# Kernel tuning notes

Measured on AMD Instinct MI355X. Metric: run time of the kernel, lower is better.

The kernel has to match this reference:

```python
import jax, jax.numpy as jnp
import numpy as np

B, Q, C = 16, 3000, 1203


def setup_inputs() -> dict:
    key = jax.random.key(0)
    k1, k2, k3, k4 = jax.random.split(key, 4)
    pred_logits = jax.random.normal(k1, (B, Q, C), dtype=jnp.float32)
    pred_boxes = jax.random.uniform(k2, (B, Q, 4), dtype=jnp.float32)
    target_sizes = jax.random.randint(k3, (B, 2), 0, 1333, dtype=jnp.int64)
    class_present = jax.random.randint(k4, (B, C), 0, 2) > 0  # bool [B, C]
    return {
        "pred_logits": pred_logits,
        "pred_boxes": pred_boxes,
        "target_sizes": target_sizes,
        "class_present": class_present,
    }


def reference(pred_logits, pred_boxes, target_sizes, class_present):
    # prob[b,q,c] = sigmoid(logits); keep if prob >= 0.5 * max_q prob[b,:,c]
    # AND class c is in targets[b]['labels'] (class_present mask).
    del target_sizes  # only shape-asserted in the original forward
    prob = jax.nn.sigmoid(pred_logits)                      # [B,Q,C]
    top = jnp.max(prob, axis=1, keepdims=True)              # [B,1,C]
    keep = (prob >= 0.5 * top) & class_present[:, None, :]   # [B,Q,C] bool
    scores = jnp.where(keep, prob, jnp.zeros((), prob.dtype))  # masked scores
    box_keep = jnp.any(keep, axis=2)                        # [B,Q] query kept for some class
    boxes = pred_boxes * box_keep[..., None].astype(pred_boxes.dtype)  # [B,Q,4]
    return scores, keep, boxes
```

## Files before the change

kernel.cpp:

```cpp
#include <hip/hip_runtime.h>
#include <math.h>

#define NB 16
#define NQR 3000
#define NC 1203

typedef float f32x4 __attribute__((ext_vector_type(4)));

__device__ __forceinline__ int lane_proc(float x, float t,
                                         float* __restrict__ s,
                                         float* __restrict__ k) {
    float pf = __builtin_amdgcn_rcpf(1.0f + __expf(-x));
    bool kp;
    float sc;
    if (pf > t + 1e-5f) {
        kp = true;  sc = pf;
    } else if (pf < t - 1e-5f) {
        kp = false; sc = 0.0f;
    } else {
        float e32 = (float)exp(-(double)x);
        float p32 = 1.0f / (1.0f + e32);
        kp = (p32 >= t);
        sc = kp ? p32 : 0.0f;
    }
    *s = sc;
    *k = kp ? 1.0f : 0.0f;
    return kp ? 1 : 0;
}

__global__ void k_partial_max(const float* __restrict__ logits,
                              float* __restrict__ partial,
                              int qc) {
    int c = blockIdx.x * blockDim.x + threadIdx.x;
    int b = blockIdx.y;
    int z = blockIdx.z;
    if (c >= NC) return;
    int q0 = z * qc;
    int q1 = min(NQR, q0 + qc);
    float m = -INFINITY;
    const float* p = logits + ((size_t)(b * NQR + q0)) * NC + c;
    int q = q0;
    for (; q + 4 <= q1; q += 4) {
        float a0 = p[0];
        float a1 = p[NC];
        float a2 = p[2 * NC];
        float a3 = p[3 * NC];
        m = fmaxf(m, fmaxf(fmaxf(a0, a1), fmaxf(a2, a3)));
        p += 4 * NC;
    }
    for (; q < q1; ++q) {
        m = fmaxf(m, *p);
        p += NC;
    }
    partial[((size_t)z * NB + b) * NC + c] = m;
}

__global__ void k_thresh(const float* __restrict__ partial,
                         const int* __restrict__ cls_present,
                         float* __restrict__ thrf,
                         int nz) {
    int c = blockIdx.x * blockDim.x + threadIdx.x;
    int b = blockIdx.y;
    if (c >= NC) return;
    float m = -INFINITY;
    for (int z = 0; z < nz; ++z)
        m = fmaxf(m, partial[((size_t)z * NB + b) * NC + c]);
    float t;
    if (cls_present[b * NC + c]) {
        float e32  = (float)exp(-(double)m);
        float ptop = 1.0f / (1.0f + e32);
        t = 0.5f * ptop;
    } else {
        t = INFINITY;
    }
    thrf[(size_t)b * NC + c] = t;
}

__global__ __launch_bounds__(256) void k_main(const float* __restrict__ logits,
                                              const float* __restrict__ boxes,
                                              const float* __restrict__ thrf,
                                              float* __restrict__ scores,
                                              float* __restrict__ keep,
                                              float* __restrict__ boxes_out) {
    int wid  = threadIdx.x >> 6;
    int lane = threadIdx.x & 63;
    int row  = blockIdx.x * 4 + wid;
    int b    = row / NQR;

    const float* lrow = logits + (size_t)row * NC;
    const float* tf   = thrf + (size_t)b * NC;
    float* srow = scores + (size_t)row * NC;
    float* krow = keep + (size_t)row * NC;

    int head = row & 3;
    int any = 0;
    float sv, kv;

    if (lane < head) {
        int c = lane;
        any |= lane_proc(lrow[c], tf[c], &sv, &kv);
        __builtin_nontemporal_store(sv, srow + c);
        __builtin_nontemporal_store(kv, krow + c);
    }

    for (int v = lane; v < 300; v += 64) {
        int c = head + 4 * v;
        f32x4 x4 = *(const f32x4*)(lrow + c);
        f32x4 s4, k4;
        float s0, s1, s2, s3, k0, k1, k2, k3;
        any |= lane_proc(x4.x, tf[c + 0], &s0, &k0);
        any |= lane_proc(x4.y, tf[c + 1], &s1, &k1);
        any |= lane_proc(x4.z, tf[c + 2], &s2, &k2);
        any |= lane_proc(x4.w, tf[c + 3], &s3, &k3);
        s4 = (f32x4){s0, s1, s2, s3};
        k4 = (f32x4){k0, k1, k2, k3};
        __builtin_nontemporal_store(s4, (f32x4*)(srow + c));
        __builtin_nontemporal_store(k4, (f32x4*)(krow + c));
    }

    if (lane < 3 - head) {
        int c = head + 1200 + lane;
        any |= lane_proc(lrow[c], tf[c], &sv, &kv);
        __builtin_nontemporal_store(sv, srow + c);
        __builtin_nontemporal_store(kv, krow + c);
    }

    unsigned long long m = __ballot(any);
    if (lane == 0) {
        float mm = m ? 1.0f : 0.0f;
        f32x4 bx = *(const f32x4*)(boxes + (size_t)row * 4);
        f32x4 o = bx * mm;
        *(f32x4*)(boxes_out + (size_t)row * 4) = o;
    }
}

extern "C" void kernel_launch(void* const* d_in, const int* in_sizes, int n_in,
                              void* d_out, int out_size, void* d_ws, size_t ws_size,
                              hipStream_t stream) {
    const float* logits      = (const float*)d_in[0];
    const float* boxes       = (const float*)d_in[1];
    const int*   cls_present = (const int*)d_in[3];

    float* scores    = (float*)d_out;
    float* keep      = scores + (size_t)NB * NQR * NC;
    float* boxes_out = keep + (size_t)NB * NQR * NC;

    int nz = 25;
    while (nz > 1 && ((size_t)nz + 1) * NB * NC * sizeof(float) > ws_size)
        nz /= 2;
    float* partial = (float*)d_ws;
    float* thrf    = partial + (size_t)nz * NB * NC;
    int qc = (NQR + nz - 1) / nz;

    dim3 gmax((NC + 255) / 256, NB, nz);
    k_partial_max<<<gmax, 256, 0, stream>>>(logits, partial, qc);

    dim3 gthr((NC + 255) / 256, NB);
    k_thresh<<<gthr, 256, 0, stream>>>(partial, cls_present, thrf, nz);

    k_main<<<(NB * NQR) / 4, 256, 0, stream>>>(logits, boxes, thrf,
                                               scores, keep, boxes_out);
}
```

Before: 190.5 us.

## Fuse column max, threshold and masking into one column-tiled kernel

Replaces the three-kernel pipeline (partial max, threshold, row-wise main pass) with one kernel per (16-column tile, batch). Each block reduces the column max over all queries in shared memory, computes thresholds, then re-reads its column strip to write scores and keep, so the second logits read can hit L2 and the extra launches disappear. The block index is remapped so consecutive column tiles land on the same XCD. Box outputs are zeroed by a separate kernel and written only for kept rows. Only 1216 blocks run, each doing scalar 64-byte-wide accesses instead of float4 rows, which risks lower bandwidth utilisation and occupancy.

```diff
diff --git a/kernel.cpp b/kernel.cpp
--- a/kernel.cpp
+++ b/kernel.cpp
@@ -28,109 +28,97 @@
     return kp ? 1 : 0;
 }
 
-__global__ void k_partial_max(const float* __restrict__ logits,
-                              float* __restrict__ partial,
-                              int qc) {
-    int c = blockIdx.x * blockDim.x + threadIdx.x;
-    int b = blockIdx.y;
-    int z = blockIdx.z;
-    if (c >= NC) return;
-    int q0 = z * qc;
-    int q1 = min(NQR, q0 + qc);
-    float m = -INFINITY;
-    const float* p = logits + ((size_t)(b * NQR + q0)) * NC + c;
-    int q = q0;
-    for (; q + 4 <= q1; q += 4) {
-        float a0 = p[0];
-        float a1 = p[NC];
-        float a2 = p[2 * NC];
-        float a3 = p[3 * NC];
-        m = fmaxf(m, fmaxf(fmaxf(a0, a1), fmaxf(a2, a3)));
-        p += 4 * NC;
-    }
-    for (; q < q1; ++q) {
-        m = fmaxf(m, *p);
-        p += NC;
-    }
-    partial[((size_t)z * NB + b) * NC + c] = m;
+__global__ void k_zero(float* __restrict__ p, int n) {
+    int i = blockIdx.x * 256 + threadIdx.x;
+    if (i < n) p[i] = 0.0f;
 }
 
-__global__ void k_thresh(const float* __restrict__ partial,
-                         const int* __restrict__ cls_present,
-                         float* __restrict__ thrf,
-                         int nz) {
-    int c = blockIdx.x * blockDim.x + threadIdx.x;
-    int b = blockIdx.y;
-    if (c >= NC) return;
+__global__ __launch_bounds__(256) void k_fused(const float* __restrict__ logits,
+                                               const float* __restrict__ boxes,
+                                               const int* __restrict__ cls_present,
+                                               float* __restrict__ scores,
+                                               float* __restrict__ keep,
+                                               float* __restrict__ boxes_out) {
+    int tid = threadIdx.x;
+    int ci  = tid & 15;
+    int qi  = tid >> 4;
+    int b   = blockIdx.y;
+
+    int ct0 = blockIdx.x;
+    int xcd = ct0 & 7, idx = ct0 >> 3;
+    int ct  = (xcd < 4) ? xcd * 10 + idx : 40 + (xcd - 4) * 9 + idx;
+
+    int c   = ct * 16 + ci;
+    bool cv = (c < NC);
+
+    const float* lcol = logits + (size_t)b * NQR * NC + c;
+
     float m = -INFINITY;
-    for (int z = 0; z < nz; ++z)
-        m = fmaxf(m, partial[((size_t)z * NB + b) * NC + c]);
-    float t;
-    if (cls_present[b * NC + c]) {
-        float e32  = (float)exp(-(double)m);
-        float ptop = 1.0f / (1.0f + e32);
-        t = 0.5f * ptop;
-    } else {
-        t = INFINITY;
-    }
-    thrf[(size_t)b * NC + c] = t;
-}
-
-__global__ __launch_bounds__(256) void k_main(const float* __restrict__ logits,
-                                              const float* __restrict__ boxes,
-                                              const float* __restrict__ thrf,
-                                              float* __restrict__ scores,
-                                              float* __restrict__ keep,
-                                              float* __restrict__ boxes_out) {
-    int wid  = threadIdx.x >> 6;
-    int lane = threadIdx.x & 63;
-    int row  = blockIdx.x * 4 + wid;
-    int b    = row / NQR;
-
-    const float* lrow = logits + (size_t)row * NC;
-    const float* tf   = thrf + (size_t)b * NC;
-    float* srow = scores + (size_t)row * NC;
-    float* krow = keep + (size_t)row * NC;
-
-    int head = row & 3;
-    int any = 0;
-    float sv, kv;
-
-    if (lane < head) {
-        int c = lane;
-        any |= lane_proc(lrow[c], tf[c], &sv, &kv);
-        __builtin_nontemporal_store(sv, srow + c);
-        __builtin_nontemporal_store(kv, krow + c);
+    if (cv) {
+        const float* p = lcol + (size_t)qi * NC;
+        int k = 0;
+        for (; k + 4 <= 184; k += 4) {
+            float a0 = p[0];
+            float a1 = p[16 * NC];
+            float a2 = p[32 * NC];
+            float a3 = p[48 * NC];
+            m = fmaxf(m, fmaxf(fmaxf(a0, a1), fmaxf(a2, a3)));
+            p += 64 * NC;
+        }
+        for (; k < 188; ++k) {
+            int q = qi + 16 * k;
+            if (q < NQR) m = fmaxf(m, *p);
+            p += 16 * NC;
+        }
     }
 
-    for (int v = lane; v < 300; v += 64) {
-        int c = head + 4 * v;
-        f32x4 x4 = *(const f32x4*)(lrow + c);
-        f32x4 s4, k4;
-        float s0, s1, s2, s3, k0, k1, k2, k3;
-        any |= lane_proc(x4.x, tf[c + 0], &s0, &k0);
-        any |= lane_proc(x4.y, tf[c + 1], &s1, &k1);
-        any |= lane_proc(x4.z, tf[c + 2], &s2, &k2);
-        any |= lane_proc(x4.w, tf[c + 3], &s3, &k3);
-        s4 = (f32x4){s0, s1, s2, s3};
-        k4 = (f32x4){k0, k1, k2, k3};
-        __builtin_nontemporal_store(s4, (f32x4*)(srow + c));
-        __builtin_nontemporal_store(k4, (f32x4*)(krow + c));
+    __shared__ float red[256];
+    __shared__ float thrs[16];
+    red[tid] = m;
+    __syncthreads();
+    if (tid < 16) {
+        float mm = red[tid];
+#pragma unroll
+        for (int j = 1; j < 16; ++j)
+            mm = fmaxf(mm, red[j * 16 + tid]);
+        int cc = ct * 16 + tid;
+        float t = INFINITY;
+        if (cc < NC && cls_present[b * NC + cc]) {
+            float e32  = (float)exp(-(double)mm);
+            float ptop = 1.0f / (1.0f + e32);
+            t = 0.5f * ptop;
+        }
+        thrs[tid] = t;
     }
+    __syncthreads();
+    float thr = thrs[ci];
 
-    if (lane < 3 - head) {
-        int c = head + 1200 + lane;
-        any |= lane_proc(lrow[c], tf[c], &sv, &kv);
-        __builtin_nontemporal_store(sv, srow + c);
-        __builtin_nontemporal_store(kv, krow + c);
-    }
+    const float* lp = lcol + (size_t)qi * NC;
+    float* sp = scores + (size_t)b * NQR * NC + c + (size_t)qi * NC;
+    float* kp = keep   + (size_t)b * NQR * NC + c + (size_t)qi * NC;
+    int gsh = (qi & 3) * 16;
 
-    unsigned long long m = __ballot(any);
-    if (lane == 0) {
-        float mm = m ? 1.0f : 0.0f;
-        f32x4 bx = *(const f32x4*)(boxes + (size_t)row * 4);
-        f32x4 o = bx * mm;
-        *(f32x4*)(boxes_out + (size_t)row * 4) = o;
+#pragma unroll 2
+    for (int k = 0; k < 188; ++k) {
+        int q = qi + 16 * k;
+        int anyk = 0;
+        bool act = cv && (q < NQR);
+        if (act) {
+            float sv, kv;
+            anyk = lane_proc(*lp, thr, &sv, &kv);
+            __builtin_nontemporal_store(sv, sp);
+            __builtin_nontemporal_store(kv, kp);
+        }
+        unsigned long long bal = __ballot(anyk);
+        unsigned rowm = (unsigned)(bal >> gsh) & 0xFFFFu;
+        if (ci == 0 && q < NQR && rowm) {
+            size_t row = (size_t)b * NQR + q;
+            f32x4 bx = *(const f32x4*)(boxes + row * 4);
+            *(f32x4*)(boxes_out + row * 4) = bx;
+        }
+        lp += 16 * NC;
+        sp += 16 * NC;
+        kp += 16 * NC;
     }
 }
 
@@ -145,19 +133,10 @@
     float* keep      = scores + (size_t)NB * NQR * NC;
     float* boxes_out = keep + (size_t)NB * NQR * NC;
 
-    int nz = 25;
-    while (nz > 1 && ((size_t)nz + 1) * NB * NC * sizeof(float) > ws_size)
-        nz /= 2;
-    float* partial = (float*)d_ws;
-    float* thrf    = partial + (size_t)nz * NB * NC;
-    int qc = (NQR + nz - 1) / nz;
+    int nbx = NB * NQR * 4;
+    k_zero<<<(nbx + 255) / 256, 256, 0, stream>>>(boxes_out, nbx);
 
-    dim3 gmax((NC + 255) / 256, NB, nz);
-    k_partial_max<<<gmax, 256, 0, stream>>>(logits, partial, qc);
-
-    dim3 gthr((NC + 255) / 256, NB);
-    k_thresh<<<gthr, 256, 0, stream>>>(partial, cls_present, thrf, nz);
-
-    k_main<<<(NB * NQR) / 4, 256, 0, stream>>>(logits, boxes, thrf,
-                                               scores, keep, boxes_out);
+    dim3 g(76, NB);
+    k_fused<<<g, 256, 0, stream>>>(logits, boxes, cls_present,
+                                   scores, keep, boxes_out);
 }
```

New measurement: 515.0 us. 170% more time.
